# Optimization experiments

Hardware: AMD Instinct MI355X
Metric: run time of the kernel (lower is better)

Reference implementation:

```python
import jax, jax.numpy as jnp
import numpy as np

NNZ = 819200
NUM_IDS = 16384
NUM_ITEMS = 100000
EMBED_DIM = 128
KPROB = 0.8  # 1 - dprob (dprob=0.2)


def setup_inputs() -> dict:
    key = jax.random.key(0)
    k1, k2, k3, k4, k5 = jax.random.split(key, 5)
    row_idx = jnp.sort(jax.random.randint(k1, (NNZ,), 0, NUM_IDS, dtype=jnp.int32))
    col_idx = jax.random.randint(k2, (NNZ,), 0, NUM_ITEMS, dtype=jnp.int32)
    data = jax.random.uniform(k3, (NNZ,), dtype=jnp.float32)
    embeddings = jax.random.normal(k4, (NUM_ITEMS, EMBED_DIM), dtype=jnp.float32)
    # Bernoulli(kprob) keep mask, matching (rand + kprob).floor().bool()
    keep_mask = jax.random.uniform(k5, (NNZ,)) < KPROB
    return {"row_idx": row_idx, "col_idx": col_idx, "data": data,
            "embeddings": embeddings, "keep_mask": keep_mask, "num_ids": NUM_IDS}


def reference(row_idx, col_idx, data, embeddings, keep_mask, num_ids):
    # Value-level sparse dropout with inverted scaling; dropped entries
    # contribute 0, so masking values is equivalent to removing nnz entries.
    val = data * keep_mask.astype(data.dtype) * (1.0 / KPROB)  # [nnz]
    # Sparse-dense matmul as gather + weighted segment-sum (embedding-bag).
    contrib = val[:, None] * embeddings[col_idx]  # [nnz, d]
    user_embeddings = jax.ops.segment_sum(contrib, row_idx, num_segments=num_ids)  # [num_ids, d]
    return user_embeddings
```

## Files before the change

kernel.cpp:

```cpp
#include <hip/hip_runtime.h>

#define NUM_IDS   16384
#define EMBED_DIM 128
#define INV_KPROB 1.25f

static __device__ __forceinline__ unsigned short f2bf(float x) {
    unsigned u = __float_as_uint(x);
    unsigned r = (u + 0x7fffu + ((u >> 16) & 1u)) >> 16;
    return (unsigned short)r;
}

__global__ void build_meta(const int*   __restrict__ row_idx,
                           const int*   __restrict__ col_idx,
                           const float* __restrict__ data,
                           const int*   __restrict__ keep,
                           int nnz,
                           int*  __restrict__ ptr,
                           int2* __restrict__ pack) {
    int i = blockIdx.x * blockDim.x + threadIdx.x;
    if (i >= nnz) return;

    const int k = keep[i];
    int2 p;
    p.x = k ? col_idx[i] : 0;
    p.y = __float_as_int(k ? data[i] * INV_KPROB : 0.0f);
    pack[i] = p;

    const int b = row_idx[i];
    if (i == 0) {
        for (int r = 0; r <= b; ++r) ptr[r] = 0;
    } else {
        const int a = row_idx[i - 1];
        for (int r = a + 1; r <= b; ++r) ptr[r] = i;
    }
    if (i == nnz - 1) {
        for (int r = b + 1; r <= NUM_IDS; ++r) ptr[r] = nnz;
    }
}

__global__ __launch_bounds__(256) void conv_bf16(const float* __restrict__ emb,
                                                 unsigned short* __restrict__ tab,
                                                 int n8) {
    int i = blockIdx.x * blockDim.x + threadIdx.x;
    if (i >= n8) return;
    const float4* src = reinterpret_cast<const float4*>(emb) + 2 * (size_t)i;
    float4 a = src[0], b = src[1];
    union { unsigned short u[8]; uint4 v; } r;
    r.u[0] = f2bf(a.x); r.u[1] = f2bf(a.y); r.u[2] = f2bf(a.z); r.u[3] = f2bf(a.w);
    r.u[4] = f2bf(b.x); r.u[5] = f2bf(b.y); r.u[6] = f2bf(b.z); r.u[7] = f2bf(b.w);
    reinterpret_cast<uint4*>(tab)[i] = r.v;
}

__global__ __launch_bounds__(256) void seg_embed_bf16(
    const int2* __restrict__ pack,
    const int*  __restrict__ ptr,
    const unsigned short* __restrict__ tab,
    float* __restrict__ out, int nnz)
{
    const int lane = threadIdx.x & 63;
    const int wave = threadIdx.x >> 6;
    const int row  = blockIdx.x * 4 + wave;
    const int qtr  = lane >> 4;
    const int pos  = lane & 15;

    const int start = __builtin_amdgcn_readfirstlane(ptr[row]);
    const int end   = __builtin_amdgcn_readfirstlane(ptr[row + 1]);

    float acc[8] = {0.f,0.f,0.f,0.f,0.f,0.f,0.f,0.f};

    for (int j = start; j < end; j += 16) {
        int   c[4];
        float v[4];
        uint4 e[4];
#pragma unroll
        for (int u = 0; u < 4; ++u) {
            const int  idx = j + 4 * u + qtr;
            const int  il  = idx < nnz ? idx : nnz - 1;
            const int2 p   = pack[il];
            const bool ok  = idx < end;
            c[u] = ok ? p.x : 0;
            v[u] = ok ? __int_as_float(p.y) : 0.0f;
        }
#pragma unroll
        for (int u = 0; u < 4; ++u) {
            e[u] = *reinterpret_cast<const uint4*>(
                       tab + (size_t)c[u] * EMBED_DIM + 8 * pos);
        }
        __builtin_amdgcn_sched_barrier(0);
#pragma unroll
        for (int u = 0; u < 4; ++u) {
#pragma unroll
            for (int k = 0; k < 4; ++k) {
                const unsigned w  = ((const unsigned*)&e[u])[k];
                const float lo = __uint_as_float(w << 16);
                const float hi = __uint_as_float(w & 0xffff0000u);
                acc[2*k]   = fmaf(v[u], lo, acc[2*k]);
                acc[2*k+1] = fmaf(v[u], hi, acc[2*k+1]);
            }
        }
    }

#pragma unroll
    for (int k = 0; k < 8; ++k) {
        acc[k] += __shfl_xor(acc[k], 16, 64);
        acc[k] += __shfl_xor(acc[k], 32, 64);
    }
    if (qtr == 0) {
        float* o = out + (size_t)row * EMBED_DIM + 8 * pos;
        *reinterpret_cast<float4*>(o)     = make_float4(acc[0], acc[1], acc[2], acc[3]);
        *reinterpret_cast<float4*>(o + 4) = make_float4(acc[4], acc[5], acc[6], acc[7]);
    }
}

__global__ __launch_bounds__(256) void seg_embed_f32(
    const int2* __restrict__ pack,
    const int*  __restrict__ ptr,
    const float* __restrict__ emb,
    float* __restrict__ out, int nnz)
{
    const int lane = threadIdx.x & 63;
    const int wave = threadIdx.x >> 6;
    const int row  = blockIdx.x * 4 + wave;
    const int half = lane >> 5;
    const int q    = lane & 31;

    const int start = __builtin_amdgcn_readfirstlane(ptr[row]);
    const int end   = __builtin_amdgcn_readfirstlane(ptr[row + 1]);

    float4 acc = make_float4(0.f, 0.f, 0.f, 0.f);

    for (int j = start; j < end; j += 8) {
        int    c[4];
        float  v[4];
        float4 e[4];
#pragma unroll
        for (int u = 0; u < 4; ++u) {
            const int  idx = j + 2 * u + half;
            const int  il  = idx < nnz ? idx : nnz - 1;
            const int2 p   = pack[il];
            const bool ok  = idx < end;
            c[u] = ok ? p.x : 0;
            v[u] = ok ? __int_as_float(p.y) : 0.0f;
        }
#pragma unroll
        for (int u = 0; u < 4; ++u) {
            e[u] = *reinterpret_cast<const float4*>(
                       emb + (size_t)c[u] * EMBED_DIM + 4 * q);
        }
        __builtin_amdgcn_sched_barrier(0);
#pragma unroll
        for (int u = 0; u < 4; ++u) {
            acc.x = fmaf(v[u], e[u].x, acc.x);
            acc.y = fmaf(v[u], e[u].y, acc.y);
            acc.z = fmaf(v[u], e[u].z, acc.z);
            acc.w = fmaf(v[u], e[u].w, acc.w);
        }
    }

    acc.x += __shfl_xor(acc.x, 32, 64);
    acc.y += __shfl_xor(acc.y, 32, 64);
    acc.z += __shfl_xor(acc.z, 32, 64);
    acc.w += __shfl_xor(acc.w, 32, 64);
    if (half == 0) {
        *reinterpret_cast<float4*>(out + (size_t)row * EMBED_DIM + 4 * q) = acc;
    }
}

extern "C" void kernel_launch(void* const* d_in, const int* in_sizes, int n_in,
                              void* d_out, int out_size, void* d_ws, size_t ws_size,
                              hipStream_t stream) {
    const int*   row_idx = (const int*)  d_in[0];
    const int*   col_idx = (const int*)  d_in[1];
    const float* data    = (const float*)d_in[2];
    const float* emb     = (const float*)d_in[3];
    const int*   keep    = (const int*)  d_in[4];
    float*       out     = (float*)d_out;
    const int    nnz     = in_sizes[0];
    const int    nitems  = in_sizes[3] / EMBED_DIM;

    const size_t ptr_bytes  = (size_t)(NUM_IDS + 1) * sizeof(int);
    const size_t pack_off   = (ptr_bytes + 255) & ~(size_t)255;
    const size_t pack_bytes = (size_t)nnz * sizeof(int2);
    const size_t tab_off    = (pack_off + pack_bytes + 255) & ~(size_t)255;
    const size_t tab_bytes  = (size_t)nitems * EMBED_DIM * sizeof(unsigned short);

    const int grid = NUM_IDS / 4;

    if (ws_size >= tab_off + tab_bytes) {
        int*            ptr  = (int*)d_ws;
        int2*           pack = (int2*)((char*)d_ws + pack_off);
        unsigned short* tab  = (unsigned short*)((char*)d_ws + tab_off);
        const int n8 = nitems * EMBED_DIM / 8;
        build_meta<<<(nnz + 255) / 256, 256, 0, stream>>>(
            row_idx, col_idx, data, keep, nnz, ptr, pack);
        conv_bf16<<<(n8 + 255) / 256, 256, 0, stream>>>(emb, tab, n8);
        seg_embed_bf16<<<grid, 256, 0, stream>>>(pack, ptr, tab, out, nnz);
    } else if (ws_size >= pack_off + pack_bytes) {
        int*  ptr  = (int*)d_ws;
        int2* pack = (int2*)((char*)d_ws + pack_off);
        build_meta<<<(nnz + 255) / 256, 256, 0, stream>>>(
            row_idx, col_idx, data, keep, nnz, ptr, pack);
        seg_embed_f32<<<grid, 256, 0, stream>>>(pack, ptr, emb, out, nnz);
    }
}
```

Baseline: 48.42 us.

## Fuse metadata build with bf16 conversion and widen gather unroll to eight

Merges the metadata kernel and the fp32-to-bf16 table conversion into one launch, with the block index selecting which job each block does. This removes one kernel launch and lets the two independent prep jobs run concurrently. The conversion now uses nontemporal loads on the fp32 embeddings. The segment gather loop handles 32 entries per iteration instead of 16, putting more loads in flight at the cost of extra registers and more masked work on short rows.

New measurement: 49.01 us. About the same (+1.2%).

```diff
diff --git a/kernel.cpp b/kernel.cpp
--- a/kernel.cpp
+++ b/kernel.cpp
@@ -3,6 +3,9 @@
 #define NUM_IDS   16384
 #define EMBED_DIM 128
 #define INV_KPROB 1.25f
+
+typedef float  fvec4 __attribute__((ext_vector_type(4)));
+typedef unsigned int uvec4 __attribute__((ext_vector_type(4)));
 
 static __device__ __forceinline__ unsigned short f2bf(float x) {
     unsigned u = __float_as_uint(x);
@@ -10,45 +13,49 @@
     return (unsigned short)r;
 }
 
-__global__ void build_meta(const int*   __restrict__ row_idx,
-                           const int*   __restrict__ col_idx,
-                           const float* __restrict__ data,
-                           const int*   __restrict__ keep,
-                           int nnz,
-                           int*  __restrict__ ptr,
-                           int2* __restrict__ pack) {
-    int i = blockIdx.x * blockDim.x + threadIdx.x;
-    if (i >= nnz) return;
-
-    const int k = keep[i];
-    int2 p;
-    p.x = k ? col_idx[i] : 0;
-    p.y = __float_as_int(k ? data[i] * INV_KPROB : 0.0f);
-    pack[i] = p;
-
-    const int b = row_idx[i];
-    if (i == 0) {
-        for (int r = 0; r <= b; ++r) ptr[r] = 0;
+__global__ __launch_bounds__(256) void prep_fused(
+    const int*   __restrict__ row_idx,
+    const int*   __restrict__ col_idx,
+    const float* __restrict__ data,
+    const int*   __restrict__ keep,
+    int nnz,
+    int*  __restrict__ ptr,
+    int2* __restrict__ pack,
+    const float* __restrict__ emb,
+    unsigned short* __restrict__ tab,
+    int n8, int nb_meta)
+{
+    if ((int)blockIdx.x < nb_meta) {
+        const int i = blockIdx.x * 256 + threadIdx.x;
+        if (i >= nnz) return;
+
+        const int k = keep[i];
+        int2 p;
+        p.x = k ? col_idx[i] : 0;
+        p.y = __float_as_int(k ? data[i] * INV_KPROB : 0.0f);
+        pack[i] = p;
+
+        const int b = row_idx[i];
+        if (i == 0) {
+            for (int r = 0; r <= b; ++r) ptr[r] = 0;
+        } else {
+            const int a = row_idx[i - 1];
+            for (int r = a + 1; r <= b; ++r) ptr[r] = i;
+        }
+        if (i == nnz - 1) {
+            for (int r = b + 1; r <= NUM_IDS; ++r) ptr[r] = nnz;
+        }
     } else {
-        const int a = row_idx[i - 1];
-        for (int r = a + 1; r <= b; ++r) ptr[r] = i;
-    }
-    if (i == nnz - 1) {
-        for (int r = b + 1; r <= NUM_IDS; ++r) ptr[r] = nnz;
-    }
-}
-
-__global__ __launch_bounds__(256) void conv_bf16(const float* __restrict__ emb,
-                                                 unsigned short* __restrict__ tab,
-                                                 int n8) {
-    int i = blockIdx.x * blockDim.x + threadIdx.x;
-    if (i >= n8) return;
-    const float4* src = reinterpret_cast<const float4*>(emb) + 2 * (size_t)i;
-    float4 a = src[0], b = src[1];
-    union { unsigned short u[8]; uint4 v; } r;
-    r.u[0] = f2bf(a.x); r.u[1] = f2bf(a.y); r.u[2] = f2bf(a.z); r.u[3] = f2bf(a.w);
-    r.u[4] = f2bf(b.x); r.u[5] = f2bf(b.y); r.u[6] = f2bf(b.z); r.u[7] = f2bf(b.w);
-    reinterpret_cast<uint4*>(tab)[i] = r.v;
+        const int i = (blockIdx.x - nb_meta) * 256 + threadIdx.x;
+        if (i >= n8) return;
+        const fvec4* src = reinterpret_cast<const fvec4*>(emb) + 2 * (size_t)i;
+        fvec4 a = __builtin_nontemporal_load(src);
+        fvec4 b = __builtin_nontemporal_load(src + 1);
+        union { unsigned short u[8]; uvec4 v; } r;
+        r.u[0] = f2bf(a.x); r.u[1] = f2bf(a.y); r.u[2] = f2bf(a.z); r.u[3] = f2bf(a.w);
+        r.u[4] = f2bf(b.x); r.u[5] = f2bf(b.y); r.u[6] = f2bf(b.z); r.u[7] = f2bf(b.w);
+        reinterpret_cast<uvec4*>(tab)[i] = r.v;
+    }
 }
 
 __global__ __launch_bounds__(256) void seg_embed_bf16(
@@ -68,12 +75,12 @@
 
     float acc[8] = {0.f,0.f,0.f,0.f,0.f,0.f,0.f,0.f};
 
-    for (int j = start; j < end; j += 16) {
-        int   c[4];
-        float v[4];
-        uint4 e[4];
-#pragma unroll
-        for (int u = 0; u < 4; ++u) {
+    for (int j = start; j < end; j += 32) {
+        int   c[8];
+        float v[8];
+        uint4 e[8];
+#pragma unroll
+        for (int u = 0; u < 8; ++u) {
             const int  idx = j + 4 * u + qtr;
             const int  il  = idx < nnz ? idx : nnz - 1;
             const int2 p   = pack[il];
@@ -82,13 +89,13 @@
             v[u] = ok ? __int_as_float(p.y) : 0.0f;
         }
 #pragma unroll
-        for (int u = 0; u < 4; ++u) {
+        for (int u = 0; u < 8; ++u) {
             e[u] = *reinterpret_cast<const uint4*>(
                        tab + (size_t)c[u] * EMBED_DIM + 8 * pos);
         }
         __builtin_amdgcn_sched_barrier(0);
 #pragma unroll
-        for (int u = 0; u < 4; ++u) {
+        for (int u = 0; u < 8; ++u) {
 #pragma unroll
             for (int k = 0; k < 4; ++k) {
                 const unsigned w  = ((const unsigned*)&e[u])[k];
@@ -184,22 +191,24 @@
     const size_t tab_off    = (pack_off + pack_bytes + 255) & ~(size_t)255;
     const size_t tab_bytes  = (size_t)nitems * EMBED_DIM * sizeof(unsigned short);
 
-    const int grid = NUM_IDS / 4;
+    const int grid    = NUM_IDS / 4;
+    const int nb_meta = (nnz + 255) / 256;
 
     if (ws_size >= tab_off + tab_bytes) {
         int*            ptr  = (int*)d_ws;
         int2*           pack = (int2*)((char*)d_ws + pack_off);
         unsigned short* tab  = (unsigned short*)((char*)d_ws + tab_off);
-        const int n8 = nitems * EMBED_DIM / 8;
-        build_meta<<<(nnz + 255) / 256, 256, 0, stream>>>(
-            row_idx, col_idx, data, keep, nnz, ptr, pack);
-        conv_bf16<<<(n8 + 255) / 256, 256, 0, stream>>>(emb, tab, n8);
+        const int n8      = nitems * EMBED_DIM / 8;
+        const int nb_conv = (n8 + 255) / 256;
+        prep_fused<<<nb_meta + nb_conv, 256, 0, stream>>>(
+            row_idx, col_idx, data, keep, nnz, ptr, pack, emb, tab, n8, nb_meta);
         seg_embed_bf16<<<grid, 256, 0, stream>>>(pack, ptr, tab, out, nnz);
     } else if (ws_size >= pack_off + pack_bytes) {
         int*  ptr  = (int*)d_ws;
         int2* pack = (int2*)((char*)d_ws + pack_off);
-        build_meta<<<(nnz + 255) / 256, 256, 0, stream>>>(
-            row_idx, col_idx, data, keep, nnz, ptr, pack);
+        prep_fused<<<nb_meta, 256, 0, stream>>>(
+            row_idx, col_idx, data, keep, nnz, ptr, pack,
+            emb, (unsigned short*)nullptr, 0, nb_meta);
         seg_embed_f32<<<grid, 256, 0, stream>>>(pack, ptr, emb, out, nnz);
     }
 }
```
